# Kernel optimization log

Measured on AMD Instinct MI355X. Metric: run time of the kernel, lower is better.

The kernel has to match this reference:

```python
import jax, jax.numpy as jnp
import numpy as np

N_NODES = 100000
N_EDGES = 1600000
N_QEDGES = 400000
NUM_FEAT = 128
HIDDEN_C = 128
OUT_C = 64
NO_HEADS = 8


def setup_inputs() -> dict:
    key = jax.random.key(0)
    ks = jax.random.split(key, 8)
    x = jax.random.normal(ks[0], (N_NODES, NUM_FEAT), dtype=jnp.float32)
    W1 = jax.random.normal(ks[1], (NUM_FEAT, HIDDEN_C), dtype=jnp.float32) * (1.0 / np.sqrt(NUM_FEAT))
    b1 = jnp.zeros((HIDDEN_C,), dtype=jnp.float32)
    W2 = jax.random.normal(ks[2], (HIDDEN_C, OUT_C * NO_HEADS), dtype=jnp.float32) * (1.0 / np.sqrt(HIDDEN_C))
    b2 = jnp.zeros((OUT_C * NO_HEADS,), dtype=jnp.float32)
    edge_index = jax.random.randint(ks[3], (2, N_EDGES), 0, N_NODES, dtype=jnp.int32)
    q_edge_index = jax.random.randint(ks[4], (2, N_QEDGES), 0, N_NODES, dtype=jnp.int32)
    y = jax.random.randint(ks[5], (N_NODES,), 0, NO_HEADS, dtype=jnp.int32)
    return {"x": x, "W1": W1, "b1": b1, "W2": W2, "b2": b2,
            "edge_index": edge_index, "q_edge_index": q_edge_index, "y": y}


def gcn_conv(x, W, b, src, dst, n):
    """GCNConv: symmetric normalization with implicit self-loops."""
    h = x @ W  # [n, out]
    ones = jnp.ones(src.shape[0], dtype=x.dtype)
    deg = jax.ops.segment_sum(ones, dst, num_segments=n) + 1.0  # self-loop
    dinv = jax.lax.rsqrt(deg)
    norm = dinv[src] * dinv[dst]  # [E]
    agg = jax.ops.segment_sum(h[src] * norm[:, None], dst, num_segments=n)
    agg = agg + h * (dinv * dinv)[:, None]  # self-loop message
    return agg + b


def reference(x, W1, b1, W2, b2, edge_index, q_edge_index, y):
    src, dst = edge_index[0], edge_index[1]
    n = x.shape[0]
    hiddens = jax.nn.relu(gcn_conv(x, W1, b1, src, dst, n))            # [N, H]
    emb = gcn_conv(hiddens, W2, b2, src, dst, n)                        # [N, heads*out]
    emb = emb.reshape(n, NO_HEADS, OUT_C)                               # [N, h, f]
    q_row, q_col = q_edge_index[0], q_edge_index[1]
    preds = jnp.einsum('ehf,ehf->eh', emb[q_row], emb[q_col])           # [Q, h]
    pred_i = jnp.take_along_axis(preds, y[q_row][:, None].astype(jnp.int32), axis=1)[:, 0]
    pred_j = jnp.take_along_axis(preds, y[q_col][:, None].astype(jnp.int32), axis=1)[:, 0]
    pred = (pred_i + pred_j) * 0.5  # multiheads=True branch
    return hiddens, emb, pred_i, pred_j, pred
```

## Files before the change

### kernel.cpp

```cpp
#include <hip/hip_runtime.h>
#include <hip/hip_bf16.h>


#define SCAN_SEG 512

typedef short bf16x8 __attribute__((ext_vector_type(8)));
typedef float f32x4  __attribute__((ext_vector_type(4)));

__device__ __forceinline__ ushort f2bf(float x) {
    return (ushort)(__float_as_uint(x) >> 16);
}
__device__ __forceinline__ float bf2f(ushort h) {
    return __uint_as_float(((unsigned)h) << 16);
}

__global__ void count_kernel(const int* __restrict__ dst, int* __restrict__ cnt, int E) {
    int e = blockIdx.x * blockDim.x + threadIdx.x;
    if (e < E) atomicAdd(&cnt[dst[e]], 1);
}

__global__ __launch_bounds__(256) void blocksum_kernel(const int* __restrict__ cnt,
                                                       int* __restrict__ blocksum, int n) {
    __shared__ int red[4];
    int b = blockIdx.x, t = threadIdx.x;
    int i0 = b * SCAN_SEG + t;
    int s = 0;
    if (i0 < n) s += cnt[i0];
    if (i0 + 256 < n) s += cnt[i0 + 256];
#pragma unroll
    for (int off = 32; off >= 1; off >>= 1) s += __shfl_xor(s, off, 64);
    if ((t & 63) == 0) red[t >> 6] = s;
    __syncthreads();
    if (t == 0) blocksum[b] = red[0] + red[1] + red[2] + red[3];
}

__global__ __launch_bounds__(256) void blockscan_kernel(const int* __restrict__ blocksum,
                                                        int* __restrict__ blockoff, int nb,
                                                        int* __restrict__ row_ptr, int n, int E) {
    __shared__ int s[256];
    int t = threadIdx.x;
    int v = (t < nb) ? blocksum[t] : 0;
    s[t] = v;
    __syncthreads();
    for (int off = 1; off < 256; off <<= 1) {
        int u = (t >= off) ? s[t - off] : 0;
        __syncthreads();
        s[t] += u;
        __syncthreads();
    }
    if (t < nb) blockoff[t] = s[t] - v;
    if (t == 0) row_ptr[n] = E;
}

__global__ __launch_bounds__(256) void csr_ptr_kernel(const int* __restrict__ cnt,
                                                      const int* __restrict__ blockoff,
                                                      int* __restrict__ row_ptr,
                                                      int* __restrict__ cursor,
                                                      float* __restrict__ dinv, int n) {
    __shared__ int s[256];
    int b = blockIdx.x, t = threadIdx.x;
    int i0 = b * SCAN_SEG + 2 * t;
    int c0 = (i0     < n) ? cnt[i0]     : 0;
    int c1 = (i0 + 1 < n) ? cnt[i0 + 1] : 0;
    int pair = c0 + c1;
    s[t] = pair;
    __syncthreads();
    for (int off = 1; off < 256; off <<= 1) {
        int u = (t >= off) ? s[t - off] : 0;
        __syncthreads();
        s[t] += u;
        __syncthreads();
    }
    int excl = s[t] - pair + blockoff[b];
    if (i0 < n) {
        row_ptr[i0] = excl;
        cursor[i0]  = excl;
        dinv[i0]    = rsqrtf((float)(c0 + 1));
    }
    if (i0 + 1 < n) {
        row_ptr[i0 + 1] = excl + c0;
        cursor[i0 + 1]  = excl + c0;
        dinv[i0 + 1]    = rsqrtf((float)(c1 + 1));
    }
}

__global__ void fill_kernel(const int* __restrict__ src, const int* __restrict__ dst,
                            int* __restrict__ cursor, const float* __restrict__ dinv,
                            int* __restrict__ csr_src, float* __restrict__ csr_wt, int E) {
    int e = blockIdx.x * blockDim.x + threadIdx.x;
    if (e < E) {
        int s = src[e], d = dst[e];
        int pos = atomicAdd(&cursor[d], 1);
        csr_src[pos] = s;
        csr_wt[pos]  = dinv[s] * dinv[d];
    }
}

__global__ __launch_bounds__(256) void wsplit_kernel(const float* __restrict__ W,
                                                     ushort* __restrict__ th,
                                                     ushort* __restrict__ tl, int ncols) {
    int idx = blockIdx.x * 256 + threadIdx.x;
    if (idx >= 128 * ncols) return;
    int col = idx >> 7;
    int k   = idx & 127;
    float v = W[(size_t)k * ncols + col];
    ushort h = f2bf(v);
    th[idx] = h;
    tl[idx] = f2bf(v - bf2f(h));
}

__global__ __launch_bounds__(256) void agg_kernel(const float* __restrict__ feat,
                                                  const int* __restrict__ row_ptr,
                                                  const int* __restrict__ csr_src,
                                                  const float* __restrict__ csr_wt,
                                                  const float* __restrict__ dinv,
                                                  ushort* __restrict__ outh,
                                                  ushort* __restrict__ outl, int n) {
    const int w    = threadIdx.x >> 6;
    const int lane = threadIdx.x & 63;
    const int node = blockIdx.x * 4 + w;
    if (node >= n) return;
    const int g = lane >> 5;
    const int c = lane & 31;

    float di = dinv[node];
    float4 acc = make_float4(0.f, 0.f, 0.f, 0.f);
    if (g == 0) {
        float4 v = ((const float4*)(feat + (size_t)node * 128))[c];
        float s2 = di * di;
        acc.x = v.x * s2; acc.y = v.y * s2; acc.z = v.z * s2; acc.w = v.w * s2;
    }

    int e0 = row_ptr[node], e1 = row_ptr[node + 1];
    int e = e0 + g;
    for (; e + 2 < e1; e += 4) {
        int   s0 = csr_src[e],  s1 = csr_src[e + 2];
        float w0 = csr_wt[e],   w1 = csr_wt[e + 2];
        float4 v0 = ((const float4*)(feat + (size_t)s0 * 128))[c];
        float4 v1 = ((const float4*)(feat + (size_t)s1 * 128))[c];
        acc.x += v0.x * w0 + v1.x * w1;
        acc.y += v0.y * w0 + v1.y * w1;
        acc.z += v0.z * w0 + v1.z * w1;
        acc.w += v0.w * w0 + v1.w * w1;
    }
    for (; e < e1; e += 2) {
        int   s0 = csr_src[e];
        float w0 = csr_wt[e];
        float4 v0 = ((const float4*)(feat + (size_t)s0 * 128))[c];
        acc.x += v0.x * w0; acc.y += v0.y * w0; acc.z += v0.z * w0; acc.w += v0.w * w0;
    }

    acc.x += __shfl_xor(acc.x, 32, 64);
    acc.y += __shfl_xor(acc.y, 32, 64);
    acc.z += __shfl_xor(acc.z, 32, 64);
    acc.w += __shfl_xor(acc.w, 32, 64);

    if (g == 0) {
        ushort4 h, l;
        h.x = f2bf(acc.x); l.x = f2bf(acc.x - bf2f(h.x));
        h.y = f2bf(acc.y); l.y = f2bf(acc.y - bf2f(h.y));
        h.z = f2bf(acc.z); l.z = f2bf(acc.z - bf2f(h.z));
        h.w = f2bf(acc.w); l.w = f2bf(acc.w - bf2f(h.w));
        *(ushort4*)(outh + (size_t)node * 128 + c * 4) = h;
        *(ushort4*)(outl + (size_t)node * 128 + c * 4) = l;
    }
}

__global__ __launch_bounds__(256, 2) void gemm_mfma(const ushort* __restrict__ Xh_g,
                                                    const ushort* __restrict__ Xl_g,
                                                    const ushort* __restrict__ Wth_g,
                                                    const ushort* __restrict__ Wtl_g,
                                                    const float* __restrict__ bias,
                                                    float* __restrict__ C,
                                                    int N, int ldw, int do_relu) {
    __shared__ ushort Xh[128 * 64];
    __shared__ ushort Xl[128 * 64];
    __shared__ ushort Wh[128 * 64];
    __shared__ ushort Wl[128 * 64];

    const int tid  = threadIdx.x;
    const int lane = tid & 63;
    const int wv   = tid >> 6;
    const int wr   = wv >> 1;
    const int wc   = wv & 1;
    const int lr   = lane & 15;
    const int lk   = lane >> 4;
    const int row0   = blockIdx.y * 128;
    const int colOff = blockIdx.x * 128;

    f32x4 acc[4][4];
#pragma unroll
    for (int i = 0; i < 4; ++i)
#pragma unroll
        for (int j = 0; j < 4; ++j)
            acc[i][j] = (f32x4){0.f, 0.f, 0.f, 0.f};

    for (int ph = 0; ph < 2; ++ph) {
        if (ph) __syncthreads();

#pragma unroll
        for (int q = 0; q < 4; ++q) {
            int cidx = tid + 256 * q;
            int row  = cidx >> 3;
            int kch  = cidx & 7;
            int gr   = row0 + row; if (gr >= N) gr = N - 1;
            size_t ge = (size_t)gr * 128 + ph * 64 + kch * 8;
            int lb = row * 128 + ((kch * 16) ^ ((row & 7) << 4));
            *(int4*)((char*)Xh + lb) = *(const int4*)(Xh_g + ge);
            *(int4*)((char*)Xl + lb) = *(const int4*)(Xl_g + ge);
        }
#pragma unroll
        for (int q = 0; q < 4; ++q) {
            int cidx = tid + 256 * q;
            int col  = cidx >> 3;
            int kch  = cidx & 7;
            size_t ge = (size_t)(colOff + col) * 128 + ph * 64 + kch * 8;
            int lb = col * 128 + ((kch * 16) ^ ((col & 7) << 4));
            *(int4*)((char*)Wh + lb) = *(const int4*)(Wth_g + ge);
            *(int4*)((char*)Wl + lb) = *(const int4*)(Wtl_g + ge);
        }
        __syncthreads();

#pragma unroll
        for (int kk = 0; kk < 2; ++kk) {
            const int kb2 = (kk * 32 + lk * 8) * 2;
            bf16x8 ah[4], al[4], bh[4], bl[4];
#pragma unroll
            for (int mi = 0; mi < 4; ++mi) {
                int row  = wr * 64 + mi * 16 + lr;
                int byte = row * 128 + (kb2 ^ ((row & 7) << 4));
                ah[mi] = *(const bf16x8*)((const char*)Xh + byte);
                al[mi] = *(const bf16x8*)((const char*)Xl + byte);
            }
#pragma unroll
            for (int ni = 0; ni < 4; ++ni) {
                int col  = wc * 64 + ni * 16 + lr;
                int byte = col * 128 + (kb2 ^ ((col & 7) << 4));
                bh[ni] = *(const bf16x8*)((const char*)Wh + byte);
                bl[ni] = *(const bf16x8*)((const char*)Wl + byte);
            }
#pragma unroll
            for (int mi = 0; mi < 4; ++mi)
#pragma unroll
                for (int ni = 0; ni < 4; ++ni) {
                    acc[mi][ni] = __builtin_amdgcn_mfma_f32_16x16x32_bf16(
                        ah[mi], bh[ni], acc[mi][ni], 0, 0, 0);
                    acc[mi][ni] = __builtin_amdgcn_mfma_f32_16x16x32_bf16(
                        ah[mi], bl[ni], acc[mi][ni], 0, 0, 0);
                    acc[mi][ni] = __builtin_amdgcn_mfma_f32_16x16x32_bf16(
                        al[mi], bh[ni], acc[mi][ni], 0, 0, 0);
                }
        }
    }

#pragma unroll
    for (int ni = 0; ni < 4; ++ni) {
        int col = colOff + wc * 64 + ni * 16 + lr;
        float bv = bias[col];
#pragma unroll
        for (int mi = 0; mi < 4; ++mi) {
            int rbase = row0 + wr * 64 + mi * 16 + (lane >> 4) * 4;
#pragma unroll
            for (int r = 0; r < 4; ++r) {
                int row = rbase + r;
                if (row < N) {
                    float v = acc[mi][ni][r] + bv;
                    if (do_relu) v = fmaxf(v, 0.f);
                    C[(size_t)row * ldw + col] = v;
                }
            }
        }
    }
}

__global__ __launch_bounds__(256) void query_kernel(const float* __restrict__ emb,
                                                    const int* __restrict__ qrow,
                                                    const int* __restrict__ qcol,
                                                    const int* __restrict__ y,
                                                    float* __restrict__ pred_i,
                                                    float* __restrict__ pred_j,
                                                    float* __restrict__ pred, int Q) {
    int wave = (int)((blockIdx.x * 256 + threadIdx.x) >> 6);
    int lane = threadIdx.x & 63;
    if (wave >= Q) return;
    int r = qrow[wave], c = qcol[wave];
    int yr = y[r], yc = y[c];
    int g = lane >> 4;
    int t = lane & 15;
    int node = (g & 1) ? c : r;
    int head = (g >> 1) ? yc : yr;
    const float4* p = (const float4*)(emb + (size_t)node * 512 + head * 64);
    float4 v = p[t];
    float4 o;
    o.x = __shfl_xor(v.x, 16, 64);
    o.y = __shfl_xor(v.y, 16, 64);
    o.z = __shfl_xor(v.z, 16, 64);
    o.w = __shfl_xor(v.w, 16, 64);
    float s = v.x * o.x + v.y * o.y + v.z * o.z + v.w * o.w;
#pragma unroll
    for (int off = 8; off >= 1; off >>= 1) s += __shfl_xor(s, off, 64);
    float other = __shfl_xor(s, 32, 64);
    if (lane == 0) {
        pred_i[wave] = s;
        pred_j[wave] = other;
        pred[wave]   = 0.5f * (s + other);
    }
}

extern "C" void kernel_launch(void* const* d_in, const int* in_sizes, int n_in,
                              void* d_out, int out_size, void* d_ws, size_t ws_size,
                              hipStream_t stream) {
    const float* x   = (const float*)d_in[0];
    const float* W1  = (const float*)d_in[1];
    const float* b1  = (const float*)d_in[2];
    const float* W2  = (const float*)d_in[3];
    const float* b2  = (const float*)d_in[4];
    const int* edge  = (const int*)d_in[5];
    const int* qedge = (const int*)d_in[6];
    const int* y     = (const int*)d_in[7];

    const int N = in_sizes[0] / 128;
    const int E = in_sizes[5] / 2;
    const int Q = in_sizes[6] / 2;

    float* out     = (float*)d_out;
    float* hiddens = out;
    float* emb     = out + (size_t)N * 128;
    float* pred_i  = emb + (size_t)N * 512;
    float* pred_j  = pred_i + Q;
    float* pred    = pred_j + Q;

    char* w = (char*)d_ws;
    auto alloc = [&](size_t bytes) { char* p = w; w += (bytes + 255) & ~(size_t)255; return p; };
    int*    cnt      = (int*)alloc((size_t)N * 4);
    int*    row_ptr  = (int*)alloc((size_t)(N + 1) * 4);
    int*    cursor   = (int*)alloc((size_t)N * 4);
    float*  dinv     = (float*)alloc((size_t)N * 4);
    int*    csr_src  = (int*)alloc((size_t)E * 4);
    float*  csr_wt   = (float*)alloc((size_t)E * 4);
    int*    blocksum = (int*)alloc(256 * 4);
    int*    blockoff = (int*)alloc(256 * 4);
    ushort* aggh     = (ushort*)alloc((size_t)N * 128 * 2);
    ushort* aggl     = (ushort*)alloc((size_t)N * 128 * 2);
    ushort* w1h      = (ushort*)alloc(128 * 128 * 2);
    ushort* w1l      = (ushort*)alloc(128 * 128 * 2);
    ushort* w2h      = (ushort*)alloc(128 * 512 * 2);
    ushort* w2l      = (ushort*)alloc(128 * 512 * 2);

    const int* esrc = edge;         const int* edst = edge + E;
    const int* qrow = qedge;        const int* qcol = qedge + Q;

    const int nb = (N + SCAN_SEG - 1) / SCAN_SEG;

    hipMemsetAsync(cnt, 0, (size_t)N * 4, stream);
    count_kernel<<<dim3((E + 255) / 256), dim3(256), 0, stream>>>(edst, cnt, E);
    blocksum_kernel<<<dim3(nb), dim3(256), 0, stream>>>(cnt, blocksum, N);
    blockscan_kernel<<<dim3(1), dim3(256), 0, stream>>>(blocksum, blockoff, nb, row_ptr, N, E);
    csr_ptr_kernel<<<dim3(nb), dim3(256), 0, stream>>>(cnt, blockoff, row_ptr, cursor, dinv, N);
    fill_kernel<<<dim3((E + 255) / 256), dim3(256), 0, stream>>>(esrc, edst, cursor, dinv, csr_src, csr_wt, E);

    wsplit_kernel<<<dim3((128 * 128 + 255) / 256), dim3(256), 0, stream>>>(W1, w1h, w1l, 128);
    wsplit_kernel<<<dim3((128 * 512 + 255) / 256), dim3(256), 0, stream>>>(W2, w2h, w2l, 512);

    const int mblocks = (N + 127) / 128;
    const int ablocks = (N + 3) / 4;

    agg_kernel<<<dim3(ablocks), dim3(256), 0, stream>>>(x, row_ptr, csr_src, csr_wt, dinv, aggh, aggl, N);
    gemm_mfma<<<dim3(1, mblocks), dim3(256), 0, stream>>>(aggh, aggl, w1h, w1l, b1, hiddens, N, 128, 1);

    agg_kernel<<<dim3(ablocks), dim3(256), 0, stream>>>(hiddens, row_ptr, csr_src, csr_wt, dinv, aggh, aggl, N);
    gemm_mfma<<<dim3(4, mblocks), dim3(256), 0, stream>>>(aggh, aggl, w2h, w2l, b2, emb, N, 512, 0);

    query_kernel<<<dim3((Q + 3) / 4), dim3(256), 0, stream>>>(emb, qrow, qcol, y, pred_i, pred_j, pred, Q);
}
```

Before: 945.8 us.

## Vectorize CSR build kernels, unroll aggregation, prefetch second GEMM K-half

The count and fill kernels now handle 4 and 2 edges per thread using vector loads, which cuts the thread count and the index-load instructions. The aggregation loop is unrolled to four gathered neighbours per half-wave so more memory loads are in flight at once. The GEMM loads the second 64-wide K half into registers while the first half is being computed, overlapping global loads with MFMA work. The costs are extra register pressure in the GEMM and in the aggregation, which could lower occupancy.

```diff
diff --git a/kernel.cpp b/kernel.cpp
--- a/kernel.cpp
+++ b/kernel.cpp
@@ -15,8 +15,16 @@
 }
 
 __global__ void count_kernel(const int* __restrict__ dst, int* __restrict__ cnt, int E) {
-    int e = blockIdx.x * blockDim.x + threadIdx.x;
-    if (e < E) atomicAdd(&cnt[dst[e]], 1);
+    int i = (blockIdx.x * blockDim.x + threadIdx.x) * 4;
+    if (i + 3 < E) {
+        int4 d = *(const int4*)(dst + i);
+        atomicAdd(&cnt[d.x], 1);
+        atomicAdd(&cnt[d.y], 1);
+        atomicAdd(&cnt[d.z], 1);
+        atomicAdd(&cnt[d.w], 1);
+    } else {
+        for (; i < E; ++i) atomicAdd(&cnt[dst[i]], 1);
+    }
 }
 
 __global__ __launch_bounds__(256) void blocksum_kernel(const int* __restrict__ cnt,
@@ -87,9 +95,18 @@
 __global__ void fill_kernel(const int* __restrict__ src, const int* __restrict__ dst,
                             int* __restrict__ cursor, const float* __restrict__ dinv,
                             int* __restrict__ csr_src, float* __restrict__ csr_wt, int E) {
-    int e = blockIdx.x * blockDim.x + threadIdx.x;
-    if (e < E) {
-        int s = src[e], d = dst[e];
+    int i = (blockIdx.x * blockDim.x + threadIdx.x) * 2;
+    if (i + 1 < E) {
+        int2 s2 = *(const int2*)(src + i);
+        int2 d2 = *(const int2*)(dst + i);
+        int p0 = atomicAdd(&cursor[d2.x], 1);
+        int p1 = atomicAdd(&cursor[d2.y], 1);
+        csr_src[p0] = s2.x;
+        csr_src[p1] = s2.y;
+        csr_wt[p0]  = dinv[s2.x] * dinv[d2.x];
+        csr_wt[p1]  = dinv[s2.y] * dinv[d2.y];
+    } else if (i < E) {
+        int s = src[i], d = dst[i];
         int pos = atomicAdd(&cursor[d], 1);
         csr_src[pos] = s;
         csr_wt[pos]  = dinv[s] * dinv[d];
@@ -133,15 +150,19 @@
 
     int e0 = row_ptr[node], e1 = row_ptr[node + 1];
     int e = e0 + g;
-    for (; e + 2 < e1; e += 4) {
-        int   s0 = csr_src[e],  s1 = csr_src[e + 2];
-        float w0 = csr_wt[e],   w1 = csr_wt[e + 2];
+    for (; e + 6 < e1; e += 8) {
+        int   s0 = csr_src[e],     s1 = csr_src[e + 2];
+        int   s2 = csr_src[e + 4], s3 = csr_src[e + 6];
+        float w0 = csr_wt[e],      w1 = csr_wt[e + 2];
+        float w2 = csr_wt[e + 4],  w3 = csr_wt[e + 6];
         float4 v0 = ((const float4*)(feat + (size_t)s0 * 128))[c];
         float4 v1 = ((const float4*)(feat + (size_t)s1 * 128))[c];
-        acc.x += v0.x * w0 + v1.x * w1;
-        acc.y += v0.y * w0 + v1.y * w1;
-        acc.z += v0.z * w0 + v1.z * w1;
-        acc.w += v0.w * w0 + v1.w * w1;
+        float4 v2 = ((const float4*)(feat + (size_t)s2 * 128))[c];
+        float4 v3 = ((const float4*)(feat + (size_t)s3 * 128))[c];
+        acc.x += v0.x * w0 + v1.x * w1 + v2.x * w2 + v3.x * w3;
+        acc.y += v0.y * w0 + v1.y * w1 + v2.y * w2 + v3.y * w3;
+        acc.z += v0.z * w0 + v1.z * w1 + v2.z * w2 + v3.z * w3;
+        acc.w += v0.w * w0 + v1.w * w1 + v2.w * w2 + v3.w * w3;
     }
     for (; e < e1; e += 2) {
         int   s0 = csr_src[e];
@@ -188,6 +209,9 @@
     const int row0   = blockIdx.y * 128;
     const int colOff = blockIdx.x * 128;
 
+    const int srow = tid >> 3;
+    const int skch = tid & 7;
+
     f32x4 acc[4][4];
 #pragma unroll
     for (int i = 0; i < 4; ++i)
@@ -195,32 +219,38 @@
         for (int j = 0; j < 4; ++j)
             acc[i][j] = (f32x4){0.f, 0.f, 0.f, 0.f};
 
-    for (int ph = 0; ph < 2; ++ph) {
-        if (ph) __syncthreads();
-
-#pragma unroll
-        for (int q = 0; q < 4; ++q) {
-            int cidx = tid + 256 * q;
-            int row  = cidx >> 3;
-            int kch  = cidx & 7;
-            int gr   = row0 + row; if (gr >= N) gr = N - 1;
-            size_t ge = (size_t)gr * 128 + ph * 64 + kch * 8;
-            int lb = row * 128 + ((kch * 16) ^ ((row & 7) << 4));
-            *(int4*)((char*)Xh + lb) = *(const int4*)(Xh_g + ge);
-            *(int4*)((char*)Xl + lb) = *(const int4*)(Xl_g + ge);
-        }
-#pragma unroll
-        for (int q = 0; q < 4; ++q) {
-            int cidx = tid + 256 * q;
-            int col  = cidx >> 3;
-            int kch  = cidx & 7;
-            size_t ge = (size_t)(colOff + col) * 128 + ph * 64 + kch * 8;
-            int lb = col * 128 + ((kch * 16) ^ ((col & 7) << 4));
-            *(int4*)((char*)Wh + lb) = *(const int4*)(Wth_g + ge);
-            *(int4*)((char*)Wl + lb) = *(const int4*)(Wtl_g + ge);
-        }
-        __syncthreads();
-
+#pragma unroll
+    for (int q = 0; q < 4; ++q) {
+        int cidx = tid + 256 * q;
+        int row  = cidx >> 3;
+        int kch  = cidx & 7;
+        int gr   = row0 + row; if (gr >= N) gr = N - 1;
+        size_t ge = (size_t)gr * 128 + kch * 8;
+        int lb = row * 128 + ((kch * 16) ^ ((row & 7) << 4));
+        *(int4*)((char*)Xh + lb) = *(const int4*)(Xh_g + ge);
+        *(int4*)((char*)Xl + lb) = *(const int4*)(Xl_g + ge);
+        size_t gw = (size_t)(colOff + row) * 128 + kch * 8;
+        *(int4*)((char*)Wh + lb) = *(const int4*)(Wth_g + gw);
+        *(int4*)((char*)Wl + lb) = *(const int4*)(Wtl_g + gw);
+    }
+    __syncthreads();
+
+    int4 pxh[4], pxl[4], pwh[4], pwl[4];
+#pragma unroll
+    for (int q = 0; q < 4; ++q) {
+        int cidx = tid + 256 * q;
+        int row  = cidx >> 3;
+        int kch  = cidx & 7;
+        int gr   = row0 + row; if (gr >= N) gr = N - 1;
+        size_t ge = (size_t)gr * 128 + 64 + kch * 8;
+        pxh[q] = *(const int4*)(Xh_g + ge);
+        pxl[q] = *(const int4*)(Xl_g + ge);
+        size_t gw = (size_t)(colOff + row) * 128 + 64 + kch * 8;
+        pwh[q] = *(const int4*)(Wth_g + gw);
+        pwl[q] = *(const int4*)(Wtl_g + gw);
+    }
+
+    auto compute64 = [&]() {
 #pragma unroll
         for (int kk = 0; kk < 2; ++kk) {
             const int kb2 = (kk * 32 + lk * 8) * 2;
@@ -251,7 +281,26 @@
                         al[mi], bh[ni], acc[mi][ni], 0, 0, 0);
                 }
         }
-    }
+    };
+
+    compute64();
+    __syncthreads();
+
+#pragma unroll
+    for (int q = 0; q < 4; ++q) {
+        int cidx = tid + 256 * q;
+        int row  = cidx >> 3;
+        int kch  = cidx & 7;
+        int lb = row * 128 + ((kch * 16) ^ ((row & 7) << 4));
+        *(int4*)((char*)Xh + lb) = pxh[q];
+        *(int4*)((char*)Xl + lb) = pxl[q];
+        *(int4*)((char*)Wh + lb) = pwh[q];
+        *(int4*)((char*)Wl + lb) = pwl[q];
+    }
+    __syncthreads();
+
+    compute64();
+    (void)srow; (void)skch;
 
 #pragma unroll
     for (int ni = 0; ni < 4; ++ni) {
@@ -353,11 +402,11 @@
     const int nb = (N + SCAN_SEG - 1) / SCAN_SEG;
 
     hipMemsetAsync(cnt, 0, (size_t)N * 4, stream);
-    count_kernel<<<dim3((E + 255) / 256), dim3(256), 0, stream>>>(edst, cnt, E);
+    count_kernel<<<dim3((E / 4 + 255) / 256), dim3(256), 0, stream>>>(edst, cnt, E);
     blocksum_kernel<<<dim3(nb), dim3(256), 0, stream>>>(cnt, blocksum, N);
     blockscan_kernel<<<dim3(1), dim3(256), 0, stream>>>(blocksum, blockoff, nb, row_ptr, N, E);
     csr_ptr_kernel<<<dim3(nb), dim3(256), 0, stream>>>(cnt, blockoff, row_ptr, cursor, dinv, N);
-    fill_kernel<<<dim3((E + 255) / 256), dim3(256), 0, stream>>>(esrc, edst, cursor, dinv, csr_src, csr_wt, E);
+    fill_kernel<<<dim3((E / 2 + 255) / 256), dim3(256), 0, stream>>>(esrc, edst, cursor, dinv, csr_src, csr_wt, E);
 
     wsplit_kernel<<<dim3((128 * 128 + 255) / 256), dim3(256), 0, stream>>>(W1, w1h, w1l, 128);
     wsplit_kernel<<<dim3((128 * 512 + 255) / 256), dim3(256), 0, stream>>>(W2, w2h, w2l, 512);
```

Result: slower. 1.035 ms (+9.4%).
